# Optimization experiments

Hardware: AMD Instinct MI355X
Metric: run time of the kernel (lower is better)

The kernel has to match this reference:

```python
import jax, jax.numpy as jnp
import numpy as np

BATCH, SEQ, DMODEL, DSTATE = 4, 2048, 1024, 16


def _hippo_legs(N):
    # HiPPO-LegS: A[n,k] = -sqrt(2n+1)sqrt(2k+1) for n>k, -(n+1) on diag; B[n]=sqrt(2n+1)
    n = np.arange(N)
    b = np.sqrt(2.0 * n + 1.0)
    A = -np.tril(np.outer(b, b), -1) - np.diag(n + 1.0)
    return A.astype(np.float32), b.astype(np.float32)


def setup_inputs() -> dict:
    key = jax.random.key(0)
    x = jax.random.normal(key, (BATCH, SEQ, DMODEL), dtype=jnp.float32)
    A_c, B_c = _hippo_legs(DSTATE)
    dt = 1.0 / float(SEQ)  # simple Euler discretization of the continuous HiPPO ODE
    A = jnp.eye(DSTATE, dtype=jnp.float32) + dt * jnp.asarray(A_c)
    Bvec = dt * jnp.asarray(B_c)
    return {"x": x, "A": A, "Bvec": Bvec}


def reference(x, A, Bvec):
    # x: (B, L, D); A: (N, N) discrete transition; Bvec: (N,) input map.
    # Selective-scan recurrence per channel: h_t = A h_{t-1} + Bvec * x_t, y_t = <Bvec, h_t>
    B, L, D = x.shape
    N = Bvec.shape[0]

    def step(h, xt):
        # h: (B, D, N), xt: (B, D)
        h = jnp.einsum('mn,bdn->bdm', A, h) + xt[..., None] * Bvec
        y = h @ Bvec  # (B, D)
        return h, y

    h0 = jnp.zeros((B, D, N), dtype=x.dtype)
    _, ys = jax.lax.scan(step, h0, jnp.moveaxis(x, 1, 0))  # ys: (L, B, D)
    return jnp.moveaxis(ys, 0, 1)  # (B, L, D)
```

## Files before the change

### kernel.cpp

```cpp
#include <hip/hip_runtime.h>

#define BATCH  4
#define SEQL   2048
#define DMODEL 1024
#define NST    16
#define CT     64
#define NCH    (SEQL / CT)
#define QSEG   16

#define WS_P     0
#define WS_W     1024
#define WS_KV    2048
#define WS_APOW  2176
#define WS_HIN   4096

__global__ __launch_bounds__(256) void setup_tables(const float* __restrict__ A,
                                                    const float* __restrict__ Bv,
                                                    float* __restrict__ ws) {
    __shared__ double buf0[256], buf1[256], buf2[256], buf3[256];
    __shared__ double bd[16], vtmp[16];
    double* S  = buf0;
    double* R  = buf1;
    double* Ta = buf2;
    double* Tb = buf3;
    const int t  = threadIdx.x;
    const int i  = t >> 4;
    const int kk = t & 15;
    const int delta = blockIdx.x;

    S[t] = (double)A[t];
    R[t] = (i == kk) ? 1.0 : 0.0;
    if (t < 16) bd[t] = (double)Bv[t];
    __syncthreads();

    for (int sb = 0; sb < 7; ++sb) {
        if ((delta >> sb) & 1) {
            double acc = 0.0;
            #pragma unroll
            for (int l = 0; l < 16; ++l) acc += R[i * 16 + l] * S[l * 16 + kk];
            Ta[t] = acc;
            __syncthreads();
            double* tmp = R; R = Ta; Ta = tmp;
        }
        if (sb < 6) {
            double acc = 0.0;
            #pragma unroll
            for (int l = 0; l < 16; ++l) acc += S[i * 16 + l] * S[l * 16 + kk];
            Tb[t] = acc;
            __syncthreads();
            double* tmp = S; S = Tb; Tb = tmp;
        }
    }

    if (delta < CT) {
        if (t < 16) {
            double acc = 0.0;
            #pragma unroll
            for (int k = 0; k < 16; ++k) acc += R[t * 16 + k] * bd[k];
            ws[WS_P + (CT - 1 - delta) * 16 + t] = (float)acc;
            vtmp[t] = acc;
        }
        __syncthreads();
        if (t == 0) {
            double kd = 0.0;
            for (int m = 0; m < 16; ++m) kd += bd[m] * vtmp[m];
            ws[WS_KV + 63 + delta] = (float)kd;
        }
    }
    if (delta >= 1 && t < 16) {
        double acc = 0.0;
        #pragma unroll
        for (int n = 0; n < 16; ++n) acc += bd[n] * R[n * 16 + t];
        ws[WS_W + (delta - 1) * 16 + t] = (float)acc;
    }
    if (delta == CT) ws[WS_APOW + t] = (float)R[t];
    if (delta == 0 && t < 63) ws[WS_KV + t] = 0.0f;
}

__global__ __launch_bounds__(256) void k1_chunkstate(const float* __restrict__ x,
                                                     const float* __restrict__ ws,
                                                     float* __restrict__ cbuf) {
    const int blk  = blockIdx.x;
    const int b    = blk >> 7;
    const int j    = (blk >> 2) & 31;
    const int dblk = blk & 3;
    const int d    = dblk * 256 + threadIdx.x;

    const float* P  = ws + WS_P;
    const float* xp = x + ((size_t)(b * SEQL + j * CT)) * DMODEL + d;

    float c[16];
    #pragma unroll
    for (int m = 0; m < 16; ++m) c[m] = 0.0f;

    float xa[8], xb[8];
    #pragma unroll
    for (int s = 0; s < 8; ++s) xa[s] = xp[(size_t)s * DMODEL];

    #pragma unroll
    for (int g = 0; g < 8; ++g) {
        float* cur = (g & 1) ? xb : xa;
        float* nxt = (g & 1) ? xa : xb;
        if (g < 7) {
            #pragma unroll
            for (int s = 0; s < 8; ++s)
                nxt[s] = xp[(size_t)((g + 1) * 8 + s) * DMODEL];
        }
        #pragma unroll
        for (int s = 0; s < 8; ++s) {
            const int ss = g * 8 + s;
            #pragma unroll
            for (int m = 0; m < 16; ++m)
                c[m] = fmaf(P[ss * 16 + m], cur[s], c[m]);
        }
    }

    float4* outp = (float4*)(cbuf + (((size_t)(b * NCH + j) * DMODEL) + d) * 16);
    #pragma unroll
    for (int q = 0; q < 4; ++q)
        outp[q] = make_float4(c[4 * q], c[4 * q + 1], c[4 * q + 2], c[4 * q + 3]);
}

__global__ __launch_bounds__(256) void k2_carry(const float* __restrict__ cbuf,
                                                float* __restrict__ ws) {
    const int blk = blockIdx.x;
    const int b   = blk >> 6;
    const int d0  = (blk & 63) * 16;
    const int t   = threadIdx.x;
    const int m   = t & 15;
    const int ch  = t >> 4;
    const int d   = d0 + ch;
    const int laneBase = t & 48;

    const size_t base0   = (((size_t)(b * NCH) * DMODEL) + d) * 16 + m;
    const size_t jstride = (size_t)DMODEL * 16;

    float cpre[NCH];
    #pragma unroll
    for (int j = 0; j < NCH; ++j)
        cpre[j] = cbuf[base0 + (size_t)j * jstride];

    float Arow[16];
    #pragma unroll
    for (int k = 0; k < 16; ++k) Arow[k] = ws[WS_APOW + m * 16 + k];

    float* hin = ws + WS_HIN;
    float s = 0.0f;
    #pragma unroll
    for (int j = 0; j < NCH; ++j) {
        hin[base0 + (size_t)j * jstride] = s;
        float acc = cpre[j];
        #pragma unroll
        for (int k = 0; k < 16; ++k)
            acc = fmaf(Arow[k], __shfl(s, laneBase + k, 64), acc);
        s = acc;
    }
}

template <int TT>
__device__ __forceinline__ void k3_body(const float* __restrict__ x,
                                        const float* __restrict__ ws,
                                        float* __restrict__ y,
                                        int b, int j, int d) {
    constexpr int LIM = (TT + 1) * QSEG;
    const float* W  = ws + WS_W + TT * QSEG * 16;
    const float* kv = ws + WS_KV;
    const float* hinp = ws + WS_HIN + (((size_t)(b * NCH + j) * DMODEL) + d) * 16;
    const float* xp = x + ((size_t)(b * SEQL + j * CT)) * DMODEL + d;

    float4 hv[4];
    #pragma unroll
    for (int q = 0; q < 4; ++q) hv[q] = ((const float4*)hinp)[q];
    float xa[8], xb[8];
    #pragma unroll
    for (int s = 0; s < 8; ++s) xa[s] = xp[(size_t)s * DMODEL];

    float h[16];
    #pragma unroll
    for (int q = 0; q < 4; ++q) {
        h[4 * q] = hv[q].x; h[4 * q + 1] = hv[q].y;
        h[4 * q + 2] = hv[q].z; h[4 * q + 3] = hv[q].w;
    }

    float yv[QSEG];
    #pragma unroll
    for (int i = 0; i < QSEG; ++i) {
        float acc = 0.0f;
        #pragma unroll
        for (int mm = 0; mm < 16; ++mm) acc = fmaf(W[i * 16 + mm], h[mm], acc);
        yv[i] = acc;
    }

    #pragma unroll
    for (int g = 0; g < LIM / 8; ++g) {
        float* cur = (g & 1) ? xb : xa;
        float* nxt = (g & 1) ? xa : xb;
        if (g + 1 < LIM / 8) {
            #pragma unroll
            for (int s = 0; s < 8; ++s)
                nxt[s] = xp[(size_t)((g + 1) * 8 + s) * DMODEL];
        }
        #pragma unroll
        for (int s = 0; s < 8; ++s) {
            const int ss = g * 8 + s;
            #pragma unroll
            for (int i = 0; i < QSEG; ++i)
                yv[i] = fmaf(kv[63 + TT * QSEG + i - ss], cur[s], yv[i]);
        }
    }

    float* yp = y + ((size_t)(b * SEQL + j * CT + TT * QSEG)) * DMODEL + d;
    #pragma unroll
    for (int i = 0; i < QSEG; ++i) yp[(size_t)i * DMODEL] = yv[i];
}

__global__ __launch_bounds__(256) void k3_output(const float* __restrict__ x,
                                                 const float* __restrict__ ws,
                                                 float* __restrict__ y) {
    const int blk  = blockIdx.x;
    const int b    = blk >> 9;
    const int j    = (blk >> 4) & 31;
    const int tt   = (blk >> 2) & 3;
    const int dblk = blk & 3;
    const int d    = dblk * 256 + threadIdx.x;

    switch (tt) {
        case 0: k3_body<0>(x, ws, y, b, j, d); break;
        case 1: k3_body<1>(x, ws, y, b, j, d); break;
        case 2: k3_body<2>(x, ws, y, b, j, d); break;
        default: k3_body<3>(x, ws, y, b, j, d); break;
    }
}

extern "C" void kernel_launch(void* const* d_in, const int* in_sizes, int n_in,
                              void* d_out, int out_size, void* d_ws, size_t ws_size,
                              hipStream_t stream) {
    (void)in_sizes; (void)n_in; (void)out_size; (void)ws_size;
    const float* x  = (const float*)d_in[0];
    const float* A  = (const float*)d_in[1];
    const float* Bv = (const float*)d_in[2];
    float* out = (float*)d_out;
    float* ws  = (float*)d_ws;

    setup_tables<<<65, 256, 0, stream>>>(A, Bv, ws);
    k1_chunkstate<<<512, 256, 0, stream>>>(x, ws, out);
    k2_carry<<<256, 256, 0, stream>>>(out, ws);
    k3_output<<<2048, 256, 0, stream>>>(x, ws, out);
}
```

Baseline: 122.8 us.

## Compute full chunk output per thread with x staged in shared memory

The output kernel now gives each thread all 64 timesteps of a chunk instead of splitting the chunk into four 16-step segments across separate blocks. The x tile is staged once into shared memory with float4 loads, so the redundant reads of earlier segments are gone and the triangular convolution work is done once. The chunk-state buffer moves from the output array to workspace. In exchange there are four times fewer blocks (512), a 64 KB shared tile limiting occupancy to about two blocks per CU, and 64 live accumulators per thread, which raises register pressure.

```diff
diff --git a/kernel.cpp b/kernel.cpp
--- a/kernel.cpp
+++ b/kernel.cpp
@@ -6,13 +6,13 @@
 #define NST    16
 #define CT     64
 #define NCH    (SEQL / CT)
-#define QSEG   16
 
 #define WS_P     0
 #define WS_W     1024
 #define WS_KV    2048
 #define WS_APOW  2176
 #define WS_HIN   4096
+#define WS_CBUF  (WS_HIN + BATCH * NCH * DMODEL * 16)
 
 __global__ __launch_bounds__(256) void setup_tables(const float* __restrict__ A,
                                                     const float* __restrict__ Bv,
@@ -78,8 +78,7 @@
 }
 
 __global__ __launch_bounds__(256) void k1_chunkstate(const float* __restrict__ x,
-                                                     const float* __restrict__ ws,
-                                                     float* __restrict__ cbuf) {
+                                                     float* __restrict__ ws) {
     const int blk  = blockIdx.x;
     const int b    = blk >> 7;
     const int j    = (blk >> 2) & 31;
@@ -115,14 +114,13 @@
         }
     }
 
-    float4* outp = (float4*)(cbuf + (((size_t)(b * NCH + j) * DMODEL) + d) * 16);
+    float4* outp = (float4*)(ws + WS_CBUF + (((size_t)(b * NCH + j) * DMODEL) + d) * 16);
     #pragma unroll
     for (int q = 0; q < 4; ++q)
         outp[q] = make_float4(c[4 * q], c[4 * q + 1], c[4 * q + 2], c[4 * q + 3]);
 }
 
-__global__ __launch_bounds__(256) void k2_carry(const float* __restrict__ cbuf,
-                                                float* __restrict__ ws) {
+__global__ __launch_bounds__(256) void k2_carry(float* __restrict__ ws) {
     const int blk = blockIdx.x;
     const int b   = blk >> 6;
     const int d0  = (blk & 63) * 16;
@@ -132,6 +130,7 @@
     const int d   = d0 + ch;
     const int laneBase = t & 48;
 
+    const float* cbuf   = ws + WS_CBUF;
     const size_t base0   = (((size_t)(b * NCH) * DMODEL) + d) * 16 + m;
     const size_t jstride = (size_t)DMODEL * 16;
 
@@ -157,79 +156,64 @@
     }
 }
 
-template <int TT>
-__device__ __forceinline__ void k3_body(const float* __restrict__ x,
-                                        const float* __restrict__ ws,
-                                        float* __restrict__ y,
-                                        int b, int j, int d) {
-    constexpr int LIM = (TT + 1) * QSEG;
-    const float* W  = ws + WS_W + TT * QSEG * 16;
-    const float* kv = ws + WS_KV;
+__global__ __launch_bounds__(256, 2) void k3_output(const float* __restrict__ x,
+                                                    const float* __restrict__ ws,
+                                                    float* __restrict__ y) {
+    __shared__ __align__(16) float xs[CT * 256];
+    const int blk  = blockIdx.x;
+    const int b    = blk >> 7;
+    const int j    = (blk >> 2) & 31;
+    const int dblk = blk & 3;
+    const int t    = threadIdx.x;
+    const int d    = dblk * 256 + t;
+
+    {
+        const float* xp = x + ((size_t)(b * SEQL + j * CT)) * DMODEL + dblk * 256;
+        const int wave = t >> 6, lane = t & 63;
+        #pragma unroll
+        for (int r = 0; r < 16; ++r) {
+            const int sigma = wave * 16 + r;
+            *(float4*)(&xs[sigma * 256 + lane * 4]) =
+                *(const float4*)(xp + (size_t)sigma * DMODEL + lane * 4);
+        }
+    }
+
     const float* hinp = ws + WS_HIN + (((size_t)(b * NCH + j) * DMODEL) + d) * 16;
-    const float* xp = x + ((size_t)(b * SEQL + j * CT)) * DMODEL + d;
-
     float4 hv[4];
     #pragma unroll
     for (int q = 0; q < 4; ++q) hv[q] = ((const float4*)hinp)[q];
-    float xa[8], xb[8];
-    #pragma unroll
-    for (int s = 0; s < 8; ++s) xa[s] = xp[(size_t)s * DMODEL];
 
     float h[16];
     #pragma unroll
     for (int q = 0; q < 4; ++q) {
-        h[4 * q] = hv[q].x; h[4 * q + 1] = hv[q].y;
+        h[4 * q]     = hv[q].x; h[4 * q + 1] = hv[q].y;
         h[4 * q + 2] = hv[q].z; h[4 * q + 3] = hv[q].w;
     }
 
-    float yv[QSEG];
-    #pragma unroll
-    for (int i = 0; i < QSEG; ++i) {
+    const float* W = ws + WS_W;
+    float yv[CT];
+    #pragma unroll
+    for (int tau = 0; tau < CT; ++tau) {
         float acc = 0.0f;
         #pragma unroll
-        for (int mm = 0; mm < 16; ++mm) acc = fmaf(W[i * 16 + mm], h[mm], acc);
-        yv[i] = acc;
-    }
-
-    #pragma unroll
-    for (int g = 0; g < LIM / 8; ++g) {
-        float* cur = (g & 1) ? xb : xa;
-        float* nxt = (g & 1) ? xa : xb;
-        if (g + 1 < LIM / 8) {
-            #pragma unroll
-            for (int s = 0; s < 8; ++s)
-                nxt[s] = xp[(size_t)((g + 1) * 8 + s) * DMODEL];
-        }
-        #pragma unroll
-        for (int s = 0; s < 8; ++s) {
-            const int ss = g * 8 + s;
-            #pragma unroll
-            for (int i = 0; i < QSEG; ++i)
-                yv[i] = fmaf(kv[63 + TT * QSEG + i - ss], cur[s], yv[i]);
-        }
-    }
-
-    float* yp = y + ((size_t)(b * SEQL + j * CT + TT * QSEG)) * DMODEL + d;
-    #pragma unroll
-    for (int i = 0; i < QSEG; ++i) yp[(size_t)i * DMODEL] = yv[i];
-}
-
-__global__ __launch_bounds__(256) void k3_output(const float* __restrict__ x,
-                                                 const float* __restrict__ ws,
-                                                 float* __restrict__ y) {
-    const int blk  = blockIdx.x;
-    const int b    = blk >> 9;
-    const int j    = (blk >> 4) & 31;
-    const int tt   = (blk >> 2) & 3;
-    const int dblk = blk & 3;
-    const int d    = dblk * 256 + threadIdx.x;
-
-    switch (tt) {
-        case 0: k3_body<0>(x, ws, y, b, j, d); break;
-        case 1: k3_body<1>(x, ws, y, b, j, d); break;
-        case 2: k3_body<2>(x, ws, y, b, j, d); break;
-        default: k3_body<3>(x, ws, y, b, j, d); break;
-    }
+        for (int m = 0; m < 16; ++m) acc = fmaf(W[tau * 16 + m], h[m], acc);
+        yv[tau] = acc;
+    }
+
+    __syncthreads();
+
+    const float* kv63 = ws + WS_KV + 63;
+    #pragma unroll
+    for (int ss = 0; ss < CT; ++ss) {
+        const float xv = xs[ss * 256 + t];
+        #pragma unroll
+        for (int q = 0; q < CT - ss; ++q)
+            yv[ss + q] = fmaf(kv63[q], xv, yv[ss + q]);
+    }
+
+    float* yp = y + ((size_t)(b * SEQL + j * CT)) * DMODEL + d;
+    #pragma unroll
+    for (int tau = 0; tau < CT; ++tau) yp[(size_t)tau * DMODEL] = yv[tau];
 }
 
 extern "C" void kernel_launch(void* const* d_in, const int* in_sizes, int n_in,
@@ -243,7 +227,7 @@
     float* ws  = (float*)d_ws;
 
     setup_tables<<<65, 256, 0, stream>>>(A, Bv, ws);
-    k1_chunkstate<<<512, 256, 0, stream>>>(x, ws, out);
-    k2_carry<<<256, 256, 0, stream>>>(out, ws);
-    k3_output<<<2048, 256, 0, stream>>>(x, ws, out);
-}
+    k1_chunkstate<<<512, 256, 0, stream>>>(x, ws);
+    k2_carry<<<256, 256, 0, stream>>>(ws);
+    k3_output<<<512, 256, 0, stream>>>(x, ws, out);
+}
```

Result: slower. 153.7 us (+25.2%).
